# Optimization experiments

Measured on AMD Instinct MI355X. Metric: run time of the kernel, lower is better.

The kernel has to match this reference:

```python
import jax, jax.numpy as jnp
import numpy as np

B, C, N, K = 4, 192, 8192, 16
C_OUT = 192


def _gather_nodes(xs, idx):
    # xs: [B, C, N], idx: [B, N, K] -> [B, C, N, K]
    return jax.vmap(lambda xb, ib: xb[:, ib])(xs, idx)


def setup_inputs() -> dict:
    key = jax.random.key(0)
    k1, k2, k3 = jax.random.split(key, 3)
    x = jax.random.normal(k1, (B, C, N, 1), dtype=jnp.float32)
    x_0 = jnp.zeros((B, C, N, 1), dtype=jnp.float32)  # unused by forward, kept for interface
    edge_index = jax.random.randint(k2, (2, B, N, K), 0, N, dtype=jnp.int32)
    # 1x1 Conv2d(2C -> C_OUT) weight flattened to [C_OUT, 2C]
    W = jax.random.normal(k3, (C_OUT, 2 * C), dtype=jnp.float32) / np.sqrt(2 * C)
    b = jnp.zeros((C_OUT,), dtype=jnp.float32)
    return {"x": x, "x_0": x_0, "edge_index": edge_index, "W": W, "b": b}


def reference(x, x_0, edge_index, W, b):
    xs = x[..., 0]                       # [B, C, N]
    x_i = _gather_nodes(xs, edge_index[1])   # centers  [B, C, N, K]
    x_j = _gather_nodes(xs, edge_index[0])   # neighbors [B, C, N, K]
    rel = jnp.max(x_j - x_i, axis=-1)        # max-relative [B, C, N]
    y = jnp.concatenate([xs, rel], axis=1)   # [B, 2C, N]
    out = jnp.einsum('oc,bcn->bon', W, y) + b[None, :, None]  # 1x1 conv
    out = jax.nn.relu(out)
    return out[..., None]                # [B, C_OUT, N, 1]
```

## Files before the change

### kernel.cpp

```cpp
#include <hip/hip_runtime.h>
#include <hip/hip_fp16.h>

#define B_    4
#define C_    192
#define N_    8192
#define K_    16
#define O_    192
#define TWOC_ 384
#define BN_   (B_ * N_)
#define NSL_  48

typedef __attribute__((ext_vector_type(8))) _Float16 half8;
typedef __attribute__((ext_vector_type(4))) _Float16 half4v;
typedef __attribute__((ext_vector_type(4))) float floatx4;
typedef __attribute__((ext_vector_type(4))) float fvec4;
typedef __attribute__((ext_vector_type(4))) int   ivec4;
typedef __attribute__((ext_vector_type(4))) unsigned int uvec4;
typedef __attribute__((ext_vector_type(2))) unsigned int uvec2;

__global__ __launch_bounds__(256) void k_prep(const float* __restrict__ x,
                                              const float* __restrict__ W,
                                              unsigned short* __restrict__ xg,
                                              unsigned short* __restrict__ Wb) {
    int bid = blockIdx.x;
    int tid = threadIdx.x;

    if (bid >= 6144) {
        int base = ((bid - 6144) * 256 + tid) * 16;
        union { unsigned short u[16]; uvec4 v[2]; } o;
#pragma unroll
        for (int q = 0; q < 16; q += 4) {
            fvec4 f = __builtin_nontemporal_load((const fvec4*)(W + base + q));
            union { _Float16 h; unsigned short s; } c;
            c.h = (_Float16)f.x; o.u[q + 0] = c.s;
            c.h = (_Float16)f.y; o.u[q + 1] = c.s;
            c.h = (_Float16)f.z; o.u[q + 2] = c.s;
            c.h = (_Float16)f.w; o.u[q + 3] = c.s;
        }
        *(uvec4*)(Wb + base)     = o.v[0];
        *(uvec4*)(Wb + base + 8) = o.v[1];
        return;
    }

    __shared__ float tile[32][33];
    int xcd  = bid & 7;
    int b    = xcd >> 1;
    int half = xcd & 1;
    int slot = bid >> 3;
    int ct   = slot >> 7;
    int nt   = half * 128 + (slot & 127);
    int c0 = ct * 32, n0 = nt * 32;

    int cc  = tid >> 3;
    int nn4 = (tid & 7) * 4;
    const float* xp = x + ((size_t)b * C_ + c0 + cc) * N_ + n0 + nn4;
    fvec4 v = __builtin_nontemporal_load((const fvec4*)xp);
    tile[nn4 + 0][cc] = v.x;
    tile[nn4 + 1][cc] = v.y;
    tile[nn4 + 2][cc] = v.z;
    tile[nn4 + 3][cc] = v.w;
    __syncthreads();

    {
        int sl  = tid >> 5;
        int row = tid & 31;
        union { _Float16 h[4]; uvec2 u; } p;
#pragma unroll
        for (int c = 0; c < 4; c++) p.h[c] = (_Float16)tile[row][sl * 4 + c];
        *(uvec2*)(xg + ((size_t)(b * NSL_ + ct * 8 + sl) * N_ + n0 + row) * 4) = p.u;
    }
}

__global__ __launch_bounds__(256) void k_gather(const unsigned short* __restrict__ xg,
                                                const int* __restrict__ eidx,
                                                unsigned short* __restrict__ rt) {
    __shared__ uvec2 lds2[N_];

    int bid  = blockIdx.x;
    int xcd  = bid & 7;
    int b    = xcd >> 1;
    int nh   = xcd & 1;
    int rest = bid >> 3;
    int s    = rest % NSL_;
    int sub  = rest / NSL_;
    int nbase = nh * 4096 + sub * 1024;
    int tid  = threadIdx.x;

    const int* e0 = eidx + (size_t)b * N_ * K_;
    const int* e1 = e0 + (size_t)BN_ * K_;

    ivec4 J[4], I[4];
    {
        const int* ej = e0 + (size_t)(nbase + tid) * K_;
        const int* ei = e1 + (size_t)(nbase + tid) * K_;
#pragma unroll
        for (int q = 0; q < 4; q++) {
            J[q] = *(const ivec4*)(ej + q * 4);
            I[q] = *(const ivec4*)(ei + q * 4);
        }
    }

    const unsigned short* src = xg + (size_t)(b * NSL_ + s) * N_ * 4;
#pragma unroll
    for (int i = 0; i < 16; i++) {
        int idx = i * 256 + tid;
        uvec4 v = *(const uvec4*)(src + (size_t)idx * 8);
        *(uvec4*)&lds2[idx * 2] = v;
    }
    __syncthreads();

    unsigned short* rto = rt + (size_t)(b * NSL_ + s) * N_ * 4;

#pragma unroll
    for (int i = 0; i < 4; i++) {
        int n = nbase + i * 256 + tid;
        ivec4 Jn[4], In[4];
        if (i < 3) {
            const int* ej = e0 + (size_t)(n + 256) * K_;
            const int* ei = e1 + (size_t)(n + 256) * K_;
#pragma unroll
            for (int q = 0; q < 4; q++) {
                Jn[q] = *(const ivec4*)(ej + q * 4);
                In[q] = *(const ivec4*)(ei + q * 4);
            }
        }
        half4v m;
#pragma unroll
        for (int q = 0; q < 4; q++)
#pragma unroll
            for (int e = 0; e < 4; e++) {
                union { uvec2 u; half4v h; } jv, iv;
                jv.u = lds2[J[q][e]];
                iv.u = lds2[I[q][e]];
                half4v d = jv.h - iv.h;
                m = (q == 0 && e == 0) ? d : __builtin_elementwise_max(m, d);
            }
        union { half4v h; uvec2 u; } o;
        o.h = m;
        *(uvec2*)(rto + (size_t)n * 4) = o.u;
#pragma unroll
        for (int q = 0; q < 4; q++) { J[q] = Jn[q]; I[q] = In[q]; }
    }
}

__global__ __launch_bounds__(256) void k_conv(const unsigned short* __restrict__ xg,
                                              const unsigned short* __restrict__ rt,
                                              const unsigned short* __restrict__ Wb,
                                              const float* __restrict__ bias,
                                              float* __restrict__ out) {
    __shared__ __align__(16) unsigned short ytile[64 * TWOC_];
    char* yb = (char*)ytile;

    int bid  = blockIdx.x;
    int xcd  = bid & 7;
    int b    = xcd >> 1;
    int slot = bid >> 3;
    int n0   = ((xcd & 1) * 64 + slot) * 64;

    int tid  = threadIdx.x;
    int wave = tid >> 6;
    int lane = tid & 63;
    int m16  = lane & 15;
    int quad = lane >> 4;

#pragma unroll
    for (int i = 0; i < 6; i++) {
        int id = i * 256 + tid;
        int s  = id >> 5;
        int np = id & 31;
        int r1 = np * 2, r2 = np * 2 + 1;
        size_t goff = ((size_t)(b * NSL_ + s) * N_ + n0 + r1) * 4;
        uvec4 vx = *(const uvec4*)(xg + goff);
        uvec4 vr = *(const uvec4*)(rt + goff);
        uvec2 x1 = {vx.x, vx.y}, x2 = {vx.z, vx.w};
        uvec2 r1v = {vr.x, vr.y}, r2v = {vr.z, vr.w};
        int sw1 = (r1 & 7) << 4, sw2 = (r2 & 7) << 4;
        *(uvec2*)(yb + r1 * 768 + ((s * 8) ^ sw1))         = x1;
        *(uvec2*)(yb + r2 * 768 + ((s * 8) ^ sw2))         = x2;
        *(uvec2*)(yb + r1 * 768 + ((384 + s * 8) ^ sw1))   = r1v;
        *(uvec2*)(yb + r2 * 768 + ((384 + s * 8) ^ sw2))   = r2v;
    }
    __syncthreads();

    const unsigned short* wbase = Wb + (size_t)(wave * 48 + m16) * TWOC_ + quad * 8;

    floatx4 acc[3][4];
#pragma unroll
    for (int i = 0; i < 3; i++)
#pragma unroll
        for (int j = 0; j < 4; j++) acc[i][j] = (floatx4){0.f, 0.f, 0.f, 0.f};

#pragma unroll 2
    for (int kt = 0; kt < 12; kt++) {
        half8 wf[3], yf[4];
#pragma unroll
        for (int i = 0; i < 3; i++)
            wf[i] = *(const half8*)(wbase + (size_t)(i * 16) * TWOC_ + kt * 32);
#pragma unroll
        for (int j = 0; j < 4; j++) {
            int row = j * 16 + m16;
            yf[j] = *(const half8*)(yb + row * 768 + ((kt * 64 + quad * 16) ^ ((row & 7) << 4)));
        }
#pragma unroll
        for (int i = 0; i < 3; i++)
#pragma unroll
            for (int j = 0; j < 4; j++)
                acc[i][j] = __builtin_amdgcn_mfma_f32_16x16x32_f16(wf[i], yf[j], acc[i][j], 0, 0, 0);
    }

#pragma unroll
    for (int i = 0; i < 3; i++) {
#pragma unroll
        for (int r = 0; r < 4; r++) {
            int o = wave * 48 + i * 16 + quad * 4 + r;
            float bv = bias[o];
#pragma unroll
            for (int j = 0; j < 4; j++) {
                int n = n0 + j * 16 + m16;
                __builtin_nontemporal_store(fmaxf(acc[i][j][r] + bv, 0.f),
                                            &out[((size_t)b * O_ + o) * N_ + n]);
            }
        }
    }
}

extern "C" void kernel_launch(void* const* d_in, const int* in_sizes, int n_in,
                              void* d_out, int out_size, void* d_ws, size_t ws_size,
                              hipStream_t stream) {
    const float* x    = (const float*)d_in[0];
    const int*   eidx = (const int*)d_in[2];
    const float* W    = (const float*)d_in[3];
    const float* bias = (const float*)d_in[4];
    float*       out  = (float*)d_out;

    unsigned short* Wb = (unsigned short*)d_ws;
    unsigned short* xg = (unsigned short*)((char*)d_ws + 147456);
    unsigned short* rt = (unsigned short*)((char*)d_ws + 12730368);

    k_prep<<<dim3(6162), dim3(256), 0, stream>>>(x, W, xg, Wb);
    k_gather<<<dim3(1536), dim3(256), 0, stream>>>(xg, eidx, rt);
    k_conv<<<dim3(512), dim3(256), 0, stream>>>(xg, rt, Wb, bias, out);
}
```

Before: 134.0 us.

## Widen channel slices from 4 to 8 halves across prep, gather and conv

After: 133.5 us (median of 2 runs). No clear change (-0.4%).

```diff
diff --git a/kernel.cpp b/kernel.cpp
--- a/kernel.cpp
+++ b/kernel.cpp
@@ -8,10 +8,9 @@
 #define O_    192
 #define TWOC_ 384
 #define BN_   (B_ * N_)
-#define NSL_  48
+#define NSL8_ 24
 
 typedef __attribute__((ext_vector_type(8))) _Float16 half8;
-typedef __attribute__((ext_vector_type(4))) _Float16 half4v;
 typedef __attribute__((ext_vector_type(4))) float floatx4;
 typedef __attribute__((ext_vector_type(4))) float fvec4;
 typedef __attribute__((ext_vector_type(4))) int   ivec4;
@@ -25,8 +24,8 @@
     int bid = blockIdx.x;
     int tid = threadIdx.x;
 
-    if (bid >= 6144) {
-        int base = ((bid - 6144) * 256 + tid) * 16;
+    if (bid >= 3072) {
+        int base = ((bid - 3072) * 256 + tid) * 16;
         union { unsigned short u[16]; uvec4 v[2]; } o;
 #pragma unroll
         for (int q = 0; q < 16; q += 4) {
@@ -42,47 +41,34 @@
         return;
     }
 
-    __shared__ float tile[32][33];
     int xcd  = bid & 7;
     int b    = xcd >> 1;
-    int half = xcd & 1;
-    int slot = bid >> 3;
-    int ct   = slot >> 7;
-    int nt   = half * 128 + (slot & 127);
-    int c0 = ct * 32, n0 = nt * 32;
-
-    int cc  = tid >> 3;
-    int nn4 = (tid & 7) * 4;
-    const float* xp = x + ((size_t)b * C_ + c0 + cc) * N_ + n0 + nn4;
-    fvec4 v = __builtin_nontemporal_load((const fvec4*)xp);
-    tile[nn4 + 0][cc] = v.x;
-    tile[nn4 + 1][cc] = v.y;
-    tile[nn4 + 2][cc] = v.z;
-    tile[nn4 + 3][cc] = v.w;
-    __syncthreads();
-
-    {
-        int sl  = tid >> 5;
-        int row = tid & 31;
-        union { _Float16 h[4]; uvec2 u; } p;
-#pragma unroll
-        for (int c = 0; c < 4; c++) p.h[c] = (_Float16)tile[row][sl * 4 + c];
-        *(uvec2*)(xg + ((size_t)(b * NSL_ + ct * 8 + sl) * N_ + n0 + row) * 4) = p.u;
-    }
-}
-
-__global__ __launch_bounds__(256) void k_gather(const unsigned short* __restrict__ xg,
-                                                const int* __restrict__ eidx,
-                                                unsigned short* __restrict__ rt) {
-    __shared__ uvec2 lds2[N_];
+    int nh   = xcd & 1;
+    int rest = bid >> 3;
+    int s    = rest >> 4;
+    int chunk= rest & 15;
+    int n    = nh * 4096 + chunk * 256 + tid;
+
+    const float* xb = x + ((size_t)b * C_ + s * 8) * N_ + n;
+    union { _Float16 h[8]; uvec4 u; } p;
+#pragma unroll
+    for (int c = 0; c < 8; c++)
+        p.h[c] = (_Float16)__builtin_nontemporal_load(xb + (size_t)c * N_);
+    *(uvec4*)(xg + ((size_t)(b * NSL8_ + s) * N_ + n) * 8) = p.u;
+}
+
+__global__ __launch_bounds__(256, 1) void k_gather(const unsigned short* __restrict__ xg,
+                                                   const int* __restrict__ eidx,
+                                                   unsigned short* __restrict__ rt) {
+    __shared__ uvec4 lds4[N_];
 
     int bid  = blockIdx.x;
     int xcd  = bid & 7;
     int b    = xcd >> 1;
     int nh   = xcd & 1;
     int rest = bid >> 3;
-    int s    = rest % NSL_;
-    int sub  = rest / NSL_;
+    int s    = rest >> 2;
+    int sub  = rest & 3;
     int nbase = nh * 4096 + sub * 1024;
     int tid  = threadIdx.x;
 
@@ -100,16 +86,15 @@
         }
     }
 
-    const unsigned short* src = xg + (size_t)(b * NSL_ + s) * N_ * 4;
-#pragma unroll
-    for (int i = 0; i < 16; i++) {
+    const unsigned short* src = xg + (size_t)(b * NSL8_ + s) * N_ * 8;
+#pragma unroll
+    for (int i = 0; i < 32; i++) {
         int idx = i * 256 + tid;
-        uvec4 v = *(const uvec4*)(src + (size_t)idx * 8);
-        *(uvec4*)&lds2[idx * 2] = v;
+        lds4[idx] = *(const uvec4*)(src + (size_t)idx * 8);
     }
     __syncthreads();
 
-    unsigned short* rto = rt + (size_t)(b * NSL_ + s) * N_ * 4;
+    unsigned short* rto = rt + (size_t)(b * NSL8_ + s) * N_ * 8;
 
 #pragma unroll
     for (int i = 0; i < 4; i++) {
@@ -124,20 +109,20 @@
                 In[q] = *(const ivec4*)(ei + q * 4);
             }
         }
-        half4v m;
+        half8 m;
 #pragma unroll
         for (int q = 0; q < 4; q++)
 #pragma unroll
             for (int e = 0; e < 4; e++) {
-                union { uvec2 u; half4v h; } jv, iv;
-                jv.u = lds2[J[q][e]];
-                iv.u = lds2[I[q][e]];
-                half4v d = jv.h - iv.h;
+                union { uvec4 u; half8 h; } jv, iv;
+                jv.u = lds4[J[q][e]];
+                iv.u = lds4[I[q][e]];
+                half8 d = jv.h - iv.h;
                 m = (q == 0 && e == 0) ? d : __builtin_elementwise_max(m, d);
             }
-        union { half4v h; uvec2 u; } o;
+        union { half8 h; uvec4 u; } o;
         o.h = m;
-        *(uvec2*)(rto + (size_t)n * 4) = o.u;
+        *(uvec4*)(rto + (size_t)n * 8) = o.u;
 #pragma unroll
         for (int q = 0; q < 4; q++) { J[q] = Jn[q]; I[q] = In[q]; }
     }
@@ -165,20 +150,15 @@
 
 #pragma unroll
     for (int i = 0; i < 6; i++) {
-        int id = i * 256 + tid;
-        int s  = id >> 5;
-        int np = id & 31;
-        int r1 = np * 2, r2 = np * 2 + 1;
-        size_t goff = ((size_t)(b * NSL_ + s) * N_ + n0 + r1) * 4;
+        int id  = i * 256 + tid;
+        int s   = id >> 6;
+        int node= id & 63;
+        size_t goff = ((size_t)(b * NSL8_ + s) * N_ + n0 + node) * 8;
         uvec4 vx = *(const uvec4*)(xg + goff);
         uvec4 vr = *(const uvec4*)(rt + goff);
-        uvec2 x1 = {vx.x, vx.y}, x2 = {vx.z, vx.w};
-        uvec2 r1v = {vr.x, vr.y}, r2v = {vr.z, vr.w};
-        int sw1 = (r1 & 7) << 4, sw2 = (r2 & 7) << 4;
-        *(uvec2*)(yb + r1 * 768 + ((s * 8) ^ sw1))         = x1;
-        *(uvec2*)(yb + r2 * 768 + ((s * 8) ^ sw2))         = x2;
-        *(uvec2*)(yb + r1 * 768 + ((384 + s * 8) ^ sw1))   = r1v;
-        *(uvec2*)(yb + r2 * 768 + ((384 + s * 8) ^ sw2))   = r2v;
+        int sw = (node & 7) << 4;
+        *(uvec4*)(yb + node * 768 + ((s * 16) ^ sw))         = vx;
+        *(uvec4*)(yb + node * 768 + ((384 + s * 16) ^ sw))   = vr;
     }
     __syncthreads();
 
@@ -237,7 +217,7 @@
     unsigned short* xg = (unsigned short*)((char*)d_ws + 147456);
     unsigned short* rt = (unsigned short*)((char*)d_ws + 12730368);
 
-    k_prep<<<dim3(6162), dim3(256), 0, stream>>>(x, W, xg, Wb);
-    k_gather<<<dim3(1536), dim3(256), 0, stream>>>(xg, eidx, rt);
+    k_prep<<<dim3(3090), dim3(256), 0, stream>>>(x, W, xg, Wb);
+    k_gather<<<dim3(768), dim3(256), 0, stream>>>(xg, eidx, rt);
     k_conv<<<dim3(512), dim3(256), 0, stream>>>(xg, rt, Wb, bias, out);
 }
```
